# Performance work log

Hardware: AMD Instinct MI355X
Metric: run time of the kernel (lower is better)

## Reference

```python
import jax, jax.numpy as jnp
import numpy as np

G = 16          # GroupNorm groups
EPS = 1e-5


def setup_inputs() -> dict:
    key = jax.random.key(0)
    ks = jax.random.split(key, 6)
    B, C, H, W = 2, 256, 96, 96
    O = 256
    x = jax.random.normal(ks[0], (B, C, H, W), dtype=jnp.float32)
    offset = jax.random.normal(ks[1], (B, 18, H, W), dtype=jnp.float32)
    mask = jax.random.uniform(ks[2], (B, 9, H, W), dtype=jnp.float32)
    fan_in = C * 9
    weight = jax.random.normal(ks[3], (O, C, 3, 3), dtype=jnp.float32) / np.sqrt(fan_in)
    bias = jnp.zeros((O,), dtype=jnp.float32)
    gamma = jnp.ones((O,), dtype=jnp.float32)
    beta = jnp.zeros((O,), dtype=jnp.float32)
    return {"x": x, "offset": offset, "mask": mask, "weight": weight,
            "bias": bias, "gamma": gamma, "beta": beta}


def _mdcn_gn(x, offset, mask, weight, bias, gamma, beta):
    B, C, H, W = x.shape
    O = weight.shape[0]
    K = 9
    # offsets: mmcv layout [y0,x0,y1,x1,...] per kernel point k = kh*3+kw
    off = offset.reshape(B, K, 2, H, W)
    off_y, off_x = off[:, :, 0], off[:, :, 1]            # [B,K,H,W]
    ky = (jnp.arange(K) // 3 - 1).astype(x.dtype)        # kernel dy, pad=1
    kx = (jnp.arange(K) % 3 - 1).astype(x.dtype)
    hh = jnp.arange(H, dtype=x.dtype)[:, None]
    ww = jnp.arange(W, dtype=x.dtype)[None, :]
    py = hh[None, None] + ky[:, None, None] + off_y      # [B,K,H,W] sample y
    px = ww[None, None] + kx[:, None, None] + off_x      # [B,K,H,W] sample x

    y0 = jnp.floor(py)
    x0 = jnp.floor(px)
    dy = py - y0
    dx = px - x0
    y0i = y0.astype(jnp.int32)
    x0i = x0.astype(jnp.int32)

    xf = x.reshape(B, C, H * W)

    def gather(yi, xi):
        # zero-padded bilinear corner: out-of-range corners contribute 0
        valid = ((yi >= 0) & (yi < H) & (xi >= 0) & (xi < W)).astype(x.dtype)
        yc = jnp.clip(yi, 0, H - 1)
        xc = jnp.clip(xi, 0, W - 1)
        idx = (yc * W + xc).reshape(B, 1, K * H * W)
        v = jnp.take_along_axis(xf, idx, axis=2).reshape(B, C, K, H, W)
        return v * valid.reshape(B, 1, K, H, W)

    w00 = ((1 - dy) * (1 - dx))[:, None]                 # [B,1,K,H,W]
    w01 = ((1 - dy) * dx)[:, None]
    w10 = (dy * (1 - dx))[:, None]
    w11 = (dy * dx)[:, None]
    val = (gather(y0i, x0i) * w00 + gather(y0i, x0i + 1) * w01 +
           gather(y0i + 1, x0i) * w10 + gather(y0i + 1, x0i + 1) * w11)
    val = val * mask[:, None]                            # modulation [B,C,K,H,W]

    out = jnp.einsum('ock,bckhw->bohw', weight.reshape(O, C, K), val)
    out = out + bias[None, :, None, None]

    # GroupNorm(16, O)
    xg = out.reshape(B, G, O // G, H, W)
    mean = xg.mean(axis=(2, 3, 4), keepdims=True)
    var = jnp.mean((xg - mean) ** 2, axis=(2, 3, 4), keepdims=True)
    xn = ((xg - mean) * jax.lax.rsqrt(var + EPS)).reshape(B, O, H, W)
    return xn * gamma[None, :, None, None] + beta[None, :, None, None]


def reference(x, offset, mask, weight, bias, gamma, beta):
    return _mdcn_gn(x, offset, mask, weight, bias, gamma, beta)
```

## Files before the change

### kernel.cpp

```cpp
#include <hip/hip_runtime.h>
#include <hip/hip_fp16.h>

typedef _Float16 f16;
typedef __attribute__((ext_vector_type(2))) _Float16 h2v;
typedef __attribute__((ext_vector_type(8))) _Float16 f16x8;
typedef __attribute__((ext_vector_type(4))) float f32x4;

#define HW_    9216
#define PADP   8
#define XP_    112
#define XPXP_  12544
#define NSTEP  72
#define NMT    288
#define XT_BYTES   12845056
#define BMAT_BYTES 1179648
#define ATILE_B    294912
#define OUTH_BYTES 9437184

#define GLOAD_LDS16(g, l) \
  __builtin_amdgcn_global_load_lds((const __attribute__((address_space(1))) void*)(g), \
                                   (__attribute__((address_space(3))) void*)(l), 16, 0, 0)

union U4 { uint4 u; h2v h[4]; f16x8 v; f16 f[8]; };
union U1 { unsigned u; h2v h; };
union UO { ushort4 s; f16 f[4]; };

__global__ __launch_bounds__(256) void k_prep_x(const float* __restrict__ x, f16* __restrict__ xT) {
    __shared__ float tile[64 * 97];
    int blk = blockIdx.x;
    int cg  = blk & 3;
    int y   = (blk >> 2) % 96;
    int b   = blk / 384;
    int t   = threadIdx.x;
    const float* src = x + (((size_t)(b*256 + cg*64))*96 + y)*96;
    for (int e = t; e < 6144; e += 256) {
        int c = e / 96, wcol = e - c*96;
        tile[c*97 + wcol] = src[(size_t)c*HW_ + wcol];
    }
    __syncthreads();
    f16* dst = xT + ((size_t)b*XPXP_ + (size_t)(y+PADP)*XP_ + PADP)*256 + cg*64;
    for (int e = t; e < 6144; e += 256) {
        int wcol = e >> 6, c = e & 63;
        dst[(size_t)wcol*256 + c] = (f16)tile[c*97 + wcol];
    }
}

__global__ __launch_bounds__(256) void k_prep_w(const float* __restrict__ wgt, f16* __restrict__ bmat) {
    int id = blockIdx.x*256 + threadIdx.x;
    int o = id / 2304;
    int rem = id - o*2304;
    int c = rem / 9;
    int k = rem - c*9;
    int s  = k*8 + (c >> 5);
    int oh = o >> 7, fn = (o >> 4) & 7, r = o & 15;
    int cp = c & 31, q = cp >> 3, e = cp & 7;
    bmat[(size_t)(s*2 + oh)*4096 + fn*512 + (q*16 + r)*8 + e] = (f16)wgt[id];
}

__global__ __launch_bounds__(256, 6) void k_sample(
        const f16* __restrict__ xT, const float* __restrict__ offs,
        const float* __restrict__ maskp, f16* __restrict__ Ag, int mt0, int nblk)
{
    __shared__ int   geo_i[64];
    __shared__ uint4 geo_w[64];

    int blk0 = blockIdx.x;
    int blk  = (blk0 & 7)*(nblk >> 3) + (blk0 >> 3);
    int mtl  = blk / 9;
    int k    = blk - mtl*9;
    int mt   = mt0 + mtl;
    int b    = mt / 144;

    int tid = threadIdx.x;
    if (tid < 64) {
        int hw = mt*64 + tid - b*HW_;
        int h = hw / 96, w = hw - h*96;
        float offy = offs[((size_t)b*18 + 2*k    )*HW_ + hw];
        float offx = offs[((size_t)b*18 + 2*k + 1)*HW_ + hw];
        float mv   = maskp[((size_t)b*9 + k)*HW_ + hw];
        int ky = k/3 - 1, kx = k - (k/3)*3 - 1;
        float py = (float)(h + ky) + offy;
        float px = (float)(w + kx) + offx;
        py = fminf(fmaxf(py, -7.5f), 102.4f);
        px = fminf(fmaxf(px, -7.5f), 102.4f);
        float y0 = floorf(py), x0 = floorf(px);
        float dy = py - y0,   dx = px - x0;
        geo_i[tid] = (((int)y0 + PADP)*XP_ + ((int)x0 + PADP)) << 9;
        float w00v = (1.f-dy)*(1.f-dx)*mv, w01v = (1.f-dy)*dx*mv;
        float w10v = dy*(1.f-dx)*mv,       w11v = dy*dx*mv;
        U1 p0, p1, p2, p3;
        p0.h = h2v{(f16)w00v, (f16)w00v};
        p1.h = h2v{(f16)w01v, (f16)w01v};
        p2.h = h2v{(f16)w10v, (f16)w10v};
        p3.h = h2v{(f16)w11v, (f16)w11v};
        geo_w[tid] = uint4{p0.u, p1.u, p2.u, p3.u};
    }
    __syncthreads();

    const char* xbC = (const char*)xT + (size_t)b*XPXP_*512;
    char* dst = (char*)Ag + (size_t)mtl*ATILE_B;

    #pragma unroll
    for (int j = 0; j < 8; ++j) {
        int item = tid + j*256;
        int row = item >> 5, chunk = item & 31;
        const char* p = xbC + geo_i[row] + (chunk << 4);
        U4 t0, t1, t2, t3, oo;
        t0.u = *(const uint4*)(p);
        t1.u = *(const uint4*)(p + 512);
        t2.u = *(const uint4*)(p + XP_*512);
        t3.u = *(const uint4*)(p + XP_*512 + 512);
        U4 w4; w4.u = geo_w[row];
        h2v w00 = w4.h[0], w01 = w4.h[1], w10 = w4.h[2], w11 = w4.h[3];
        #pragma unroll
        for (int q = 0; q < 4; ++q)
            oo.h[q] = w00*t0.h[q] + w01*t1.h[q] + w10*t2.h[q] + w11*t3.h[q];
        int s = k*8 + (chunk >> 2);
        int off = ((row >> 4) << 10) + (((row & 15) + ((chunk & 3) << 4)) << 4);
        *(uint4*)(dst + (size_t)s*4096 + off) = oo.u;
    }
}

__global__ __launch_bounds__(256, 4) void k_gemm(
        const f16* __restrict__ Ag, const f16* __restrict__ bmat,
        const float* __restrict__ bias, f16* __restrict__ outh,
        float* __restrict__ part, int mt0, int nblk)
{
    __shared__ __align__(16) char LDS[3*12288];
    __shared__ float psum[2][8][2];

    int blk0 = blockIdx.x;
    int blk  = (blk0 & 7)*(nblk >> 3) + (blk0 >> 3);
    int mtl  = blk >> 1;
    int oh   = blk & 1;
    int mt   = mt0 + mtl;

    int tid = threadIdx.x, lane = tid & 63, wid = tid >> 6;
    int wm = wid >> 1, wn = wid & 1;

    const char* aG = (const char*)Ag + (size_t)mtl*ATILE_B;
    const char* bG = (const char*)bmat + (oh << 13);
    char* ldsC = &LDS[0];

    f32x4 acc[2][4];
    #pragma unroll
    for (int i = 0; i < 2; ++i)
        #pragma unroll
        for (int j = 0; j < 4; ++j) acc[i][j] = (f32x4){0.f,0.f,0.f,0.f};

#define STAGE(t_, BUF) do { \
    const char* ga_ = aG + ((size_t)(t_) << 12); \
    GLOAD_LDS16(ga_ + (tid << 4),            ldsC + (BUF)*12288 + (tid << 4)); \
    const char* gb_ = bG + ((size_t)(t_) << 14); \
    GLOAD_LDS16(gb_ + (tid << 4),            ldsC + (BUF)*12288 + 4096 + (tid << 4)); \
    GLOAD_LDS16(gb_ + 4096 + (tid << 4),     ldsC + (BUF)*12288 + 8192 + (tid << 4)); \
  } while (0)

#define MM(CUR) do { \
    const char* Lc_ = ldsC + (CUR)*12288; \
    f16x8 a0_ = *(const f16x8*)(Lc_ + ((wm*2 + 0) << 10) + (lane << 4)); \
    f16x8 a1_ = *(const f16x8*)(Lc_ + ((wm*2 + 1) << 10) + (lane << 4)); \
    _Pragma("unroll") \
    for (int j_ = 0; j_ < 4; ++j_) { \
      f16x8 bf_ = *(const f16x8*)(Lc_ + 4096 + ((wn*4 + j_) << 10) + (lane << 4)); \
      acc[0][j_] = __builtin_amdgcn_mfma_f32_16x16x32_f16(a0_, bf_, acc[0][j_], 0, 0, 0); \
      acc[1][j_] = __builtin_amdgcn_mfma_f32_16x16x32_f16(a1_, bf_, acc[1][j_], 0, 0, 0); \
    } \
  } while (0)

#define ITER(s_, CUR, NBUF, PF, VN) do { \
    asm volatile("s_waitcnt vmcnt(" VN ")" ::: "memory"); \
    __builtin_amdgcn_s_barrier(); \
    __builtin_amdgcn_sched_barrier(0); \
    if (PF) STAGE((s_)+2, NBUF); \
    __builtin_amdgcn_s_setprio(1); \
    MM(CUR); \
    __builtin_amdgcn_s_setprio(0); \
  } while (0)

    STAGE(0, 0);
    STAGE(1, 1);
    for (int sb = 0; sb < 69; sb += 3) {
        ITER(sb,   0, 2, 1, "3");
        ITER(sb+1, 1, 0, 1, "3");
        ITER(sb+2, 2, 1, 1, "3");
    }
    ITER(69, 0, 2, 1, "3");
    ITER(70, 1, 0, 0, "3");
    ITER(71, 2, 1, 0, "0");

#undef STAGE
#undef MM
#undef ITER

    int ol = lane & 15;
    int qr = (lane >> 4) << 2;
    int b  = mt / 144;
    int hwb = mt*64 - b*HW_;
    #pragma unroll
    for (int fm = 0; fm < 2; ++fm) {
        int mrow = wm*32 + fm*16 + qr;
        #pragma unroll
        for (int j = 0; j < 4; ++j) {
            int o = oh*128 + wn*64 + j*16 + ol;
            float bv = bias[o];
            f32x4 a = acc[fm][j];
            a[0] += bv; a[1] += bv; a[2] += bv; a[3] += bv;
            acc[fm][j] = a;
            UO ov;
            ov.f[0] = (f16)a[0]; ov.f[1] = (f16)a[1];
            ov.f[2] = (f16)a[2]; ov.f[3] = (f16)a[3];
            *(ushort4*)(outh + ((size_t)(b*256 + o))*HW_ + hwb + mrow) = ov.s;
        }
    }
    #pragma unroll
    for (int j = 0; j < 4; ++j) {
        float s1 = 0.f, s2 = 0.f;
        #pragma unroll
        for (int fm = 0; fm < 2; ++fm) {
            f32x4 a = acc[fm][j];
            s1 += a[0]+a[1]+a[2]+a[3];
            s2 += a[0]*a[0]+a[1]*a[1]+a[2]*a[2]+a[3]*a[3];
        }
        #pragma unroll
        for (int m = 32; m > 0; m >>= 1) {
            s1 += __shfl_xor(s1, m);
            s2 += __shfl_xor(s2, m);
        }
        if (lane == 0) { psum[wm][wn*4+j][0] = s1; psum[wm][wn*4+j][1] = s2; }
    }
    __syncthreads();
    if (tid < 8) {
        float s1 = psum[0][tid][0] + psum[1][tid][0];
        float s2 = psum[0][tid][1] + psum[1][tid][1];
        part[(size_t)(mt*2 + oh)*16 + tid*2]     = s1;
        part[(size_t)(mt*2 + oh)*16 + tid*2 + 1] = s2;
    }
}

__global__ __launch_bounds__(256) void k_finalize(const float* __restrict__ part, float* __restrict__ stats) {
    int bg = blockIdx.x, b = bg >> 4, g = bg & 15;
    int oh = g >> 3, gl = g & 7;
    float s1 = 0.f, s2 = 0.f;
    if (threadIdx.x < 144) {
        int mt = b*144 + threadIdx.x;
        const float* p = part + (size_t)(mt*2 + oh)*16 + gl*2;
        s1 = p[0]; s2 = p[1];
    }
    __shared__ float a1[256], a2[256];
    a1[threadIdx.x] = s1; a2[threadIdx.x] = s2;
    __syncthreads();
    for (int off = 128; off > 0; off >>= 1) {
        if (threadIdx.x < off) { a1[threadIdx.x] += a1[threadIdx.x+off]; a2[threadIdx.x] += a2[threadIdx.x+off]; }
        __syncthreads();
    }
    if (threadIdx.x == 0) {
        float inv_n = 1.f/147456.f;
        float mean = a1[0]*inv_n;
        float var  = fmaxf(a2[0]*inv_n - mean*mean, 0.f);
        stats[bg*2]   = mean;
        stats[bg*2+1] = rsqrtf(var + 1e-5f);
    }
}

__global__ __launch_bounds__(256) void k_norm(const f16* __restrict__ outh, float* __restrict__ out,
                                              const float* __restrict__ stats,
                                              const float* __restrict__ gamma, const float* __restrict__ beta) {
    int i8 = blockIdx.x*256 + threadIdx.x;
    int p  = i8 / 1152;
    int o  = p & 255;
    float mean = stats[(p>>4)*2], rstd = stats[(p>>4)*2 + 1];
    float ga = gamma[o]*rstd, be = beta[o] - mean*rstd*gamma[o];
    U4 v; v.u = ((const uint4*)outh)[i8];
    float4 o0, o1;
    o0.x = (float)v.f[0]*ga + be; o0.y = (float)v.f[1]*ga + be;
    o0.z = (float)v.f[2]*ga + be; o0.w = (float)v.f[3]*ga + be;
    o1.x = (float)v.f[4]*ga + be; o1.y = (float)v.f[5]*ga + be;
    o1.z = (float)v.f[6]*ga + be; o1.w = (float)v.f[7]*ga + be;
    ((float4*)out)[i8*2]     = o0;
    ((float4*)out)[i8*2 + 1] = o1;
}

extern "C" void kernel_launch(void* const* d_in, const int* in_sizes, int n_in,
                              void* d_out, int out_size, void* d_ws, size_t ws_size,
                              hipStream_t stream) {
    const float* x      = (const float*)d_in[0];
    const float* offset = (const float*)d_in[1];
    const float* mask   = (const float*)d_in[2];
    const float* weight = (const float*)d_in[3];
    const float* bias   = (const float*)d_in[4];
    const float* gamma  = (const float*)d_in[5];
    const float* beta   = (const float*)d_in[6];
    float* out = (float*)d_out;

    char* ws = (char*)d_ws;
    f16*   xT    = (f16*)ws;
    f16*   bmat  = (f16*)(ws + XT_BYTES);
    float* part  = (float*)(ws + XT_BYTES + BMAT_BYTES);
    float* stats = (float*)(ws + XT_BYTES + BMAT_BYTES + 36864);
    f16*   outh  = (f16*)(ws + 14061824);
    char*  Ag    = ws + 14061824 + OUTH_BYTES;

    size_t needA = (size_t)NMT * ATILE_B;
    size_t base  = 14061824 + (size_t)OUTH_BYTES;
    size_t avail = ws_size > base ? ws_size - base : 0;
    int P = (avail >= needA) ? 1 : ((avail >= needA/2) ? 2 : 4);

    (void)hipMemsetAsync(xT, 0, XT_BYTES, stream);
    k_prep_x<<<768, 256, 0, stream>>>(x, xT);
    k_prep_w<<<2304, 256, 0, stream>>>(weight, bmat);
    int mtn = NMT / P;
    for (int p = 0; p < P; ++p) {
        k_sample<<<mtn*9, 256, 0, stream>>>(xT, offset, mask, (f16*)Ag, p*mtn, mtn*9);
        k_gemm<<<mtn*2, 256, 0, stream>>>((f16*)Ag, bmat, bias, outh, part, p*mtn, mtn*2);
    }
    k_finalize<<<32, 256, 0, stream>>>(part, stats);
    k_norm<<<2304, 256, 0, stream>>>(outh, out, stats, gamma, beta);
}
```

Before: 94.71 us.

## Replace LDS-staged GEMM with single-wave blocks loading fragments directly from global

The GEMM kernel drops LDS staging and barriers. Each 64-thread block now computes a 32x64 output tile, streaming MFMA fragments straight from global memory into registers with a three-deep register prefetch. The sample and weight-prep kernels write A and B in the matching per-wave fragment layout, and partial stats are stored at finer granularity for finalize to sum. This removes LDS round-trips and block-wide sync, but operands that were shared across waves in LDS are now fetched separately by each wave, which raises L2/global traffic.

```diff
diff --git a/kernel.cpp b/kernel.cpp
--- a/kernel.cpp
+++ b/kernel.cpp
@@ -16,10 +16,7 @@
 #define BMAT_BYTES 1179648
 #define ATILE_B    294912
 #define OUTH_BYTES 9437184
-
-#define GLOAD_LDS16(g, l) \
-  __builtin_amdgcn_global_load_lds((const __attribute__((address_space(1))) void*)(g), \
-                                   (__attribute__((address_space(3))) void*)(l), 16, 0, 0)
+#define PART_BYTES 73728
 
 union U4 { uint4 u; h2v h[4]; f16x8 v; f16 f[8]; };
 union U1 { unsigned u; h2v h; };
@@ -52,9 +49,9 @@
     int c = rem / 9;
     int k = rem - c*9;
     int s  = k*8 + (c >> 5);
-    int oh = o >> 7, fn = (o >> 4) & 7, r = o & 15;
-    int cp = c & 31, q = cp >> 3, e = cp & 7;
-    bmat[(size_t)(s*2 + oh)*4096 + fn*512 + (q*16 + r)*8 + e] = (f16)wgt[id];
+    int nw = o >> 6, fn = (o >> 4) & 3, r = o & 15;
+    int kq = (c >> 3) & 3, e = c & 7;
+    bmat[(size_t)s*8192 + nw*2048 + fn*512 + (kq*16 + r)*8 + e] = (f16)wgt[id];
 }
 
 __global__ __launch_bounds__(256, 6) void k_sample(
@@ -116,31 +113,45 @@
         for (int q = 0; q < 4; ++q)
             oo.h[q] = w00*t0.h[q] + w01*t1.h[q] + w10*t2.h[q] + w11*t3.h[q];
         int s = k*8 + (chunk >> 2);
-        int off = ((row >> 4) << 10) + (((row & 15) + ((chunk & 3) << 4)) << 4);
-        *(uint4*)(dst + (size_t)s*4096 + off) = oo.u;
-    }
-}
-
-__global__ __launch_bounds__(256, 4) void k_gemm(
+        size_t off = (size_t)(row >> 5)*147456 + (size_t)s*2048
+                   + ((row >> 4) & 1)*1024 + (((chunk & 3)*16 + (row & 15)) << 4);
+        *(uint4*)(dst + off) = oo.u;
+    }
+}
+
+#define MFMA16(a,b,c) __builtin_amdgcn_mfma_f32_16x16x32_f16(a,b,c,0,0,0)
+
+#define LOADS(A0,A1,B0,B1,B2,B3, s_) do { \
+    const char* pa_ = aB + (size_t)(s_)*2048; \
+    const char* pb_ = bB + (size_t)(s_)*16384; \
+    A0 = *(const uint4*)(pa_); \
+    A1 = *(const uint4*)(pa_ + 1024); \
+    B0 = *(const uint4*)(pb_); \
+    B1 = *(const uint4*)(pb_ + 1024); \
+    B2 = *(const uint4*)(pb_ + 2048); \
+    B3 = *(const uint4*)(pb_ + 3072); \
+  } while (0)
+
+#define MMS(A0,A1,B0,B1,B2,B3) do { \
+    U4 xa0, xa1, xb; xa0.u = A0; xa1.u = A1; \
+    xb.u = B0; acc[0][0] = MFMA16(xa0.v, xb.v, acc[0][0]); acc[1][0] = MFMA16(xa1.v, xb.v, acc[1][0]); \
+    xb.u = B1; acc[0][1] = MFMA16(xa0.v, xb.v, acc[0][1]); acc[1][1] = MFMA16(xa1.v, xb.v, acc[1][1]); \
+    xb.u = B2; acc[0][2] = MFMA16(xa0.v, xb.v, acc[0][2]); acc[1][2] = MFMA16(xa1.v, xb.v, acc[1][2]); \
+    xb.u = B3; acc[0][3] = MFMA16(xa0.v, xb.v, acc[0][3]); acc[1][3] = MFMA16(xa1.v, xb.v, acc[1][3]); \
+  } while (0)
+
+__global__ __launch_bounds__(64) void k_gemm(
         const f16* __restrict__ Ag, const f16* __restrict__ bmat,
         const float* __restrict__ bias, f16* __restrict__ outh,
-        float* __restrict__ part, int mt0, int nblk)
+        float* __restrict__ part, int mt0, int nwv)
 {
-    __shared__ __align__(16) char LDS[3*12288];
-    __shared__ float psum[2][8][2];
-
-    int blk0 = blockIdx.x;
-    int blk  = (blk0 & 7)*(nblk >> 3) + (blk0 >> 3);
-    int mtl  = blk >> 1;
-    int oh   = blk & 1;
-    int mt   = mt0 + mtl;
-
-    int tid = threadIdx.x, lane = tid & 63, wid = tid >> 6;
-    int wm = wid >> 1, wn = wid & 1;
-
-    const char* aG = (const char*)Ag + (size_t)mtl*ATILE_B;
-    const char* bG = (const char*)bmat + (oh << 13);
-    char* ldsC = &LDS[0];
+    int w0 = blockIdx.x;
+    int w  = (w0 & 7)*(nwv >> 3) + (w0 >> 3);
+    int mw = w >> 2, nw = w & 3;
+    int lane = threadIdx.x;
+
+    const char* aB = (const char*)Ag + (size_t)mw*147456 + lane*16;
+    const char* bB = (const char*)bmat + nw*4096 + lane*16;
 
     f32x4 acc[2][4];
     #pragma unroll
@@ -148,77 +159,49 @@
         #pragma unroll
         for (int j = 0; j < 4; ++j) acc[i][j] = (f32x4){0.f,0.f,0.f,0.f};
 
-#define STAGE(t_, BUF) do { \
-    const char* ga_ = aG + ((size_t)(t_) << 12); \
-    GLOAD_LDS16(ga_ + (tid << 4),            ldsC + (BUF)*12288 + (tid << 4)); \
-    const char* gb_ = bG + ((size_t)(t_) << 14); \
-    GLOAD_LDS16(gb_ + (tid << 4),            ldsC + (BUF)*12288 + 4096 + (tid << 4)); \
-    GLOAD_LDS16(gb_ + 4096 + (tid << 4),     ldsC + (BUF)*12288 + 8192 + (tid << 4)); \
-  } while (0)
-
-#define MM(CUR) do { \
-    const char* Lc_ = ldsC + (CUR)*12288; \
-    f16x8 a0_ = *(const f16x8*)(Lc_ + ((wm*2 + 0) << 10) + (lane << 4)); \
-    f16x8 a1_ = *(const f16x8*)(Lc_ + ((wm*2 + 1) << 10) + (lane << 4)); \
-    _Pragma("unroll") \
-    for (int j_ = 0; j_ < 4; ++j_) { \
-      f16x8 bf_ = *(const f16x8*)(Lc_ + 4096 + ((wn*4 + j_) << 10) + (lane << 4)); \
-      acc[0][j_] = __builtin_amdgcn_mfma_f32_16x16x32_f16(a0_, bf_, acc[0][j_], 0, 0, 0); \
-      acc[1][j_] = __builtin_amdgcn_mfma_f32_16x16x32_f16(a1_, bf_, acc[1][j_], 0, 0, 0); \
-    } \
-  } while (0)
-
-#define ITER(s_, CUR, NBUF, PF, VN) do { \
-    asm volatile("s_waitcnt vmcnt(" VN ")" ::: "memory"); \
-    __builtin_amdgcn_s_barrier(); \
-    __builtin_amdgcn_sched_barrier(0); \
-    if (PF) STAGE((s_)+2, NBUF); \
-    __builtin_amdgcn_s_setprio(1); \
-    MM(CUR); \
-    __builtin_amdgcn_s_setprio(0); \
-  } while (0)
-
-    STAGE(0, 0);
-    STAGE(1, 1);
-    for (int sb = 0; sb < 69; sb += 3) {
-        ITER(sb,   0, 2, 1, "3");
-        ITER(sb+1, 1, 0, 1, "3");
-        ITER(sb+2, 2, 1, 1, "3");
-    }
-    ITER(69, 0, 2, 1, "3");
-    ITER(70, 1, 0, 0, "3");
-    ITER(71, 2, 1, 0, "0");
-
-#undef STAGE
-#undef MM
-#undef ITER
-
-    int ol = lane & 15;
-    int qr = (lane >> 4) << 2;
-    int b  = mt / 144;
-    int hwb = mt*64 - b*HW_;
+    uint4 a00,a01,b00,b01,b02,b03;
+    uint4 a10,a11,b10,b11,b12,b13;
+    uint4 a20,a21,b20,b21,b22,b23;
+
+    LOADS(a00,a01,b00,b01,b02,b03, 0);
+    LOADS(a10,a11,b10,b11,b12,b13, 1);
+    LOADS(a20,a21,b20,b21,b22,b23, 2);
+
+    for (int s = 0; s < 69; s += 3) {
+        MMS(a00,a01,b00,b01,b02,b03);  LOADS(a00,a01,b00,b01,b02,b03, s+3);
+        MMS(a10,a11,b10,b11,b12,b13);  LOADS(a10,a11,b10,b11,b12,b13, s+4);
+        MMS(a20,a21,b20,b21,b22,b23);  LOADS(a20,a21,b20,b21,b22,b23, s+5);
+    }
+    MMS(a00,a01,b00,b01,b02,b03);
+    MMS(a10,a11,b10,b11,b12,b13);
+    MMS(a20,a21,b20,b21,b22,b23);
+
+    int mwg = mt0*2 + mw;
+    int b   = mwg / 288;
+    int hwb = mwg*32 - b*HW_;
+    int ol  = lane & 15;
+    int qr  = (lane >> 4) << 2;
     #pragma unroll
     for (int fm = 0; fm < 2; ++fm) {
-        int mrow = wm*32 + fm*16 + qr;
-        #pragma unroll
-        for (int j = 0; j < 4; ++j) {
-            int o = oh*128 + wn*64 + j*16 + ol;
+        #pragma unroll
+        for (int fn = 0; fn < 4; ++fn) {
+            int o = nw*64 + fn*16 + ol;
             float bv = bias[o];
-            f32x4 a = acc[fm][j];
+            f32x4 a = acc[fm][fn];
             a[0] += bv; a[1] += bv; a[2] += bv; a[3] += bv;
-            acc[fm][j] = a;
+            acc[fm][fn] = a;
             UO ov;
             ov.f[0] = (f16)a[0]; ov.f[1] = (f16)a[1];
             ov.f[2] = (f16)a[2]; ov.f[3] = (f16)a[3];
-            *(ushort4*)(outh + ((size_t)(b*256 + o))*HW_ + hwb + mrow) = ov.s;
-        }
-    }
-    #pragma unroll
-    for (int j = 0; j < 4; ++j) {
+            *(ushort4*)(outh + ((size_t)(b*256 + o))*HW_ + hwb + fm*16 + qr) = ov.s;
+        }
+    }
+    #pragma unroll
+    for (int fn = 0; fn < 4; ++fn) {
         float s1 = 0.f, s2 = 0.f;
         #pragma unroll
         for (int fm = 0; fm < 2; ++fm) {
-            f32x4 a = acc[fm][j];
+            f32x4 a = acc[fm][fn];
             s1 += a[0]+a[1]+a[2]+a[3];
             s2 += a[0]*a[0]+a[1]*a[1]+a[2]*a[2]+a[3]*a[3];
         }
@@ -227,25 +210,19 @@
             s1 += __shfl_xor(s1, m);
             s2 += __shfl_xor(s2, m);
         }
-        if (lane == 0) { psum[wm][wn*4+j][0] = s1; psum[wm][wn*4+j][1] = s2; }
-    }
-    __syncthreads();
-    if (tid < 8) {
-        float s1 = psum[0][tid][0] + psum[1][tid][0];
-        float s2 = psum[0][tid][1] + psum[1][tid][1];
-        part[(size_t)(mt*2 + oh)*16 + tid*2]     = s1;
-        part[(size_t)(mt*2 + oh)*16 + tid*2 + 1] = s2;
+        if (lane == 0) {
+            part[((size_t)mwg*16 + nw*4 + fn)*2]     = s1;
+            part[((size_t)mwg*16 + nw*4 + fn)*2 + 1] = s2;
+        }
     }
 }
 
 __global__ __launch_bounds__(256) void k_finalize(const float* __restrict__ part, float* __restrict__ stats) {
     int bg = blockIdx.x, b = bg >> 4, g = bg & 15;
-    int oh = g >> 3, gl = g & 7;
     float s1 = 0.f, s2 = 0.f;
-    if (threadIdx.x < 144) {
-        int mt = b*144 + threadIdx.x;
-        const float* p = part + (size_t)(mt*2 + oh)*16 + gl*2;
-        s1 = p[0]; s2 = p[1];
+    for (int j = threadIdx.x; j < 288; j += 256) {
+        const float* p = part + ((size_t)(b*288 + j)*16 + g)*2;
+        s1 += p[0]; s2 += p[1];
     }
     __shared__ float a1[256], a2[256];
     a1[threadIdx.x] = s1; a2[threadIdx.x] = s2;
@@ -297,12 +274,12 @@
     f16*   xT    = (f16*)ws;
     f16*   bmat  = (f16*)(ws + XT_BYTES);
     float* part  = (float*)(ws + XT_BYTES + BMAT_BYTES);
-    float* stats = (float*)(ws + XT_BYTES + BMAT_BYTES + 36864);
-    f16*   outh  = (f16*)(ws + 14061824);
-    char*  Ag    = ws + 14061824 + OUTH_BYTES;
+    float* stats = (float*)(ws + XT_BYTES + BMAT_BYTES + PART_BYTES);
+    f16*   outh  = (f16*)(ws + XT_BYTES + BMAT_BYTES + PART_BYTES + 256);
+    char*  Ag    = ws + XT_BYTES + BMAT_BYTES + PART_BYTES + 256 + OUTH_BYTES;
 
     size_t needA = (size_t)NMT * ATILE_B;
-    size_t base  = 14061824 + (size_t)OUTH_BYTES;
+    size_t base  = (size_t)XT_BYTES + BMAT_BYTES + PART_BYTES + 256 + OUTH_BYTES;
     size_t avail = ws_size > base ? ws_size - base : 0;
     int P = (avail >= needA) ? 1 : ((avail >= needA/2) ? 2 : 4);
 
@@ -312,7 +289,7 @@
     int mtn = NMT / P;
     for (int p = 0; p < P; ++p) {
         k_sample<<<mtn*9, 256, 0, stream>>>(xT, offset, mask, (f16*)Ag, p*mtn, mtn*9);
-        k_gemm<<<mtn*2, 256, 0, stream>>>((f16*)Ag, bmat, bias, outh, part, p*mtn, mtn*2);
+        k_gemm<<<mtn*8, 64, 0, stream>>>((f16*)Ag, bmat, bias, outh, part, p*mtn, mtn*8);
     }
     k_finalize<<<32, 256, 0, stream>>>(part, stats);
     k_norm<<<2304, 256, 0, stream>>>(outh, out, stats, gamma, beta);
```

Measured after the change: 97.57 us. +3.0%, slower.
